# Optimization experiments

Measured on AMD Instinct MI355X. Metric: run time of the kernel, lower is better.

The kernel has to match this reference:

```python
import jax, jax.numpy as jnp
import numpy as np

B, C, H, W, NP = 4, 512, 32, 32, 2048
NH = 4
EPS = 1e-5


def setup_inputs() -> dict:
    key = jax.random.key(0)
    ks = jax.random.split(key, 12)
    s = 0.02
    d = {}
    d["img_feature"] = jax.random.normal(ks[0], (B, C, H, W), jnp.float32)
    d["point_feature"] = jax.random.normal(ks[1], (B, C, NP), jnp.float32)
    d["mlp_w1"] = jax.random.normal(ks[2], (2 * C, C), jnp.float32) * s
    d["mlp_b1"] = jnp.zeros((2 * C,), jnp.float32)
    d["bn1_gamma"] = jnp.ones((2 * C,), jnp.float32)
    d["bn1_beta"] = jnp.zeros((2 * C,), jnp.float32)
    d["bn1_mean"] = jnp.zeros((2 * C,), jnp.float32)
    d["bn1_var"] = jnp.ones((2 * C,), jnp.float32)
    d["mlp_w2"] = jax.random.normal(ks[3], (C, 2 * C), jnp.float32) * s
    d["mlp_b2"] = jnp.zeros((C,), jnp.float32)
    d["bn2_gamma"] = jnp.ones((C,), jnp.float32)
    d["bn2_beta"] = jnp.zeros((C,), jnp.float32)
    d["bn2_mean"] = jnp.zeros((C,), jnp.float32)
    d["bn2_var"] = jnp.ones((C,), jnp.float32)
    d["attn_qw"] = jax.random.normal(ks[4], (3, C, C), jnp.float32) * s
    d["attn_qb"] = jnp.zeros((3, C), jnp.float32)
    d["attn_kw"] = jax.random.normal(ks[5], (3, C, C), jnp.float32) * s
    d["attn_kb"] = jnp.zeros((3, C), jnp.float32)
    d["attn_vw"] = jax.random.normal(ks[6], (3, C, C), jnp.float32) * s
    d["attn_vb"] = jnp.zeros((3, C), jnp.float32)
    d["attn_ln_g"] = jnp.ones((3, C), jnp.float32)
    d["attn_ln_b"] = jnp.zeros((3, C), jnp.float32)
    return d


def _bn(x, g, b, m, v):  # x: [B, C, N], eval-mode batchnorm over channel dim
    return (x - m[:, None]) * jax.lax.rsqrt(v[:, None] + EPS) * g[:, None] + b[:, None]


def _mlp(x, w1, b1, g1, be1, m1, v1, w2, b2, g2, be2, m2, v2):
    # 1x1 Conv1d == per-position linear over channels
    y = jnp.einsum('oc,bcn->bon', w1, x) + b1[:, None]
    y = jax.nn.relu(_bn(y, g1, be1, m1, v1))
    z = jnp.einsum('oc,bcn->bon', w2, y) + b2[:, None]
    return jax.nn.relu(_bn(z, g2, be2, m2, v2))


def _self_attn(x, qw, qb, kw, kb, vw, vb, lng, lnb):
    # x: [B, S, E]; NOTE: original scales by 1/sqrt(hidden_size), not head_dim
    Bq, S, E = x.shape
    Hd = E // NH
    q = (jnp.einsum('bse,de->bsd', x, qw) + qb).reshape(Bq, S, NH, Hd)
    k = (jnp.einsum('bse,de->bsd', x, kw) + kb).reshape(Bq, S, NH, Hd)
    v = (jnp.einsum('bse,de->bsd', x, vw) + vb).reshape(Bq, S, NH, Hd)
    scores = jnp.einsum('bqhd,bkhd->bhqk', q, k) * (float(E) ** -0.5)
    attn = jax.nn.softmax(scores, axis=-1)
    out = jnp.einsum('bhqk,bkhd->bqhd', attn, v).reshape(Bq, S, E)
    y = out + x
    mu = jnp.mean(y, axis=-1, keepdims=True)
    var = jnp.var(y, axis=-1, keepdims=True)
    return (y - mu) * jax.lax.rsqrt(var + EPS) * lng + lnb


def reference(img_feature, point_feature, mlp_w1, mlp_b1, bn1_gamma, bn1_beta,
              bn1_mean, bn1_var, mlp_w2, mlp_b2, bn2_gamma, bn2_beta, bn2_mean,
              bn2_var, attn_qw, attn_qb, attn_kw, attn_kb, attn_vw, attn_vb,
              attn_ln_g, attn_ln_b):
    b, c, h, w = img_feature.shape
    i_in = img_feature.reshape(b, c, h * w)  # [B, C, N_i]
    mlp_args = (mlp_w1, mlp_b1, bn1_gamma, bn1_beta, bn1_mean, bn1_var,
                mlp_w2, mlp_b2, bn2_gamma, bn2_beta, bn2_mean, bn2_var)
    p_feat = _mlp(point_feature, *mlp_args)  # [B, C, N_p]
    i_feat = _mlp(i_in, *mlp_args)           # [B, C, N_i]
    phi = jnp.einsum('bcp,bci->bpi', p_feat, i_feat) * (float(c) ** -0.5)
    phi_p = jax.nn.softmax(phi, axis=1)   # softmax over points
    phi_i = jax.nn.softmax(phi, axis=-1)  # softmax over image positions
    I_enh = jnp.einsum('bcp,bpi->bci', p_feat, phi_p)  # [B, C, N_i]
    P_enh = jnp.einsum('bci,bpi->bcp', i_feat, phi_i)  # [B, C, N_p]
    att = lambda x, j: _self_attn(x, attn_qw[j], attn_qb[j], attn_kw[j],
                                  attn_kb[j], attn_vw[j], attn_vb[j],
                                  attn_ln_g[j], attn_ln_b[j])
    I = att(jnp.swapaxes(I_enh, 1, 2), 0)  # [B, N_i, C]
    P = att(jnp.swapaxes(P_enh, 1, 2), 1)  # [B, N_p, C]
    joint = jnp.concatenate([P, I], axis=1)  # [B, N_p + N_i, C]
    return att(joint, 2)
```

## Files before the change

### kernel.cpp

```cpp
#include <hip/hip_runtime.h>
#include <math.h>

#define LN_EPS 1e-5f

typedef __attribute__((ext_vector_type(8))) short bf16x8;
typedef __attribute__((ext_vector_type(4))) float f32x4;

#define GLDS16(g, l) __builtin_amdgcn_global_load_lds( \
    (const __attribute__((address_space(1))) unsigned int*)(g), \
    (__attribute__((address_space(3))) unsigned int*)(l), 16, 0, 0)

__device__ __forceinline__ float b2f(unsigned short h) { return __uint_as_float(((unsigned)h) << 16); }
__device__ __forceinline__ unsigned short f2b(float f) {
  unsigned u = __float_as_uint(f);
  unsigned r = (u + 0x7fffu + ((u >> 16) & 1u)) >> 16;
  return (unsigned short)r;
}
__device__ __forceinline__ float ld(const float* p) { return *p; }
__device__ __forceinline__ float ld(const unsigned short* p) { return b2f(*p); }
__device__ __forceinline__ void st(float* p, float v) { *p = v; }
__device__ __forceinline__ void st(unsigned short* p, float v) { *p = f2b(v); }

__device__ __forceinline__ float bred_sum(float v, float* red) {
  for (int o = 32; o; o >>= 1) v += __shfl_down(v, o, 64);
  int wid = threadIdx.x >> 6;
  __syncthreads();
  if ((threadIdx.x & 63) == 0) red[wid] = v;
  __syncthreads();
  return red[0] + red[1] + red[2] + red[3];
}

__global__ void prep_all(
    const float* __restrict__ w1, const float* __restrict__ w2, const float* __restrict__ vw,
    const float* __restrict__ qw, const float* __restrict__ qb,
    const float* __restrict__ kw, const float* __restrict__ kb,
    const float* __restrict__ b1, const float* __restrict__ g1, const float* __restrict__ be1,
    const float* __restrict__ m1, const float* __restrict__ v1,
    const float* __restrict__ b2, const float* __restrict__ g2, const float* __restrict__ be2,
    const float* __restrict__ m2, const float* __restrict__ v2,
    unsigned short* __restrict__ w1b, unsigned short* __restrict__ w2b,
    unsigned short* __restrict__ vwb, unsigned short* __restrict__ qkw,
    float* __restrict__ qkbias, float* __restrict__ s1, float* __restrict__ f1,
    float* __restrict__ s2, float* __restrict__ f2)
{
  const float scl = 0.044194173824159216f * 1.4426950408889634f;
  int idx = blockIdx.x * 256 + threadIdx.x;
  {
    int j = idx >> 19; int r = idx & 524287; int n = r >> 9; int k = r & 511;
    float v = (n < 512) ? qw[j * 262144 + n * 512 + k] * scl
                        : kw[j * 262144 + (n - 512) * 512 + k];
    qkw[idx] = f2b(v);
  }
  if (idx < 524288) { w1b[idx] = f2b(w1[idx]); w2b[idx] = f2b(w2[idx]); }
  if (idx < 786432) vwb[idx] = f2b(vw[idx]);
  if (idx < 3072) {
    int j = idx >> 10, n = idx & 1023;
    qkbias[idx] = (n < 512) ? qb[j * 512 + n] * scl : kb[j * 512 + n - 512];
  }
  if (idx < 1024) { float s = g1[idx] * rsqrtf(v1[idx] + LN_EPS); s1[idx] = s; f1[idx] = (b1[idx] - m1[idx]) * s + be1[idx]; }
  if (idx < 512)  { float s = g2[idx] * rsqrtf(v2[idx] + LN_EPS); s2[idx] = s; f2[idx] = (b2[idx] - m2[idx]) * s + be2[idx]; }
}

template<typename TS, typename TD>
__global__ __launch_bounds__(256) void transpose_t(const TS* __restrict__ src,
    TD* __restrict__ dst, int R, int Cc, long sS, long sD) {
  __shared__ float t[32][33];
  src += (long)blockIdx.z * sS; dst += (long)blockIdx.z * sD;
  int c0 = blockIdx.x * 32, r0 = blockIdx.y * 32;
  int tx = threadIdx.x & 31, ty = threadIdx.x >> 5;
#pragma unroll
  for (int rr = 0; rr < 32; rr += 8) t[ty + rr][tx] = ld(&src[(long)(r0 + ty + rr) * Cc + c0 + tx]);
  __syncthreads();
#pragma unroll
  for (int rr = 0; rr < 32; rr += 8) st(&dst[(long)(c0 + ty + rr) * R + r0 + tx], t[tx][ty + rr]);
}

template<int PER>
__global__ __launch_bounds__(256) void softmax_k(const float* __restrict__ x,
    unsigned short* __restrict__ y, long bstr) {
  __shared__ float red[4];
  const int L = PER * 256;
  int b = blockIdx.y, r = blockIdx.x, tid = threadIdx.x;
  const float* p = x + (long)b * bstr + (long)r * L;
  unsigned short* o = y + (long)b * bstr + (long)r * L;
  float vals[PER];
  float mx = -1e30f;
#pragma unroll
  for (int t = 0; t < PER; t++) { float v = p[tid + (t << 8)]; vals[t] = v; mx = fmaxf(mx, v); }
  for (int ofs = 32; ofs; ofs >>= 1) mx = fmaxf(mx, __shfl_down(mx, ofs, 64));
  int wid = tid >> 6;
  if ((tid & 63) == 0) red[wid] = mx;
  __syncthreads();
  mx = fmaxf(fmaxf(red[0], red[1]), fmaxf(red[2], red[3]));
  float sm = 0.f;
#pragma unroll
  for (int t = 0; t < PER; t++) { float e = __expf(vals[t] - mx); vals[t] = e; sm += e; }
  sm = bred_sum(sm, red);
  float inv = 1.f / sm;
#pragma unroll
  for (int t = 0; t < PER; t++) o[tid + (t << 8)] = f2b(vals[t] * inv);
}

template<int EPI, typename TC>
__global__ __launch_bounds__(256) void gemm_bf16(
    const unsigned short* __restrict__ A, long sA, int lda,
    const unsigned short* __restrict__ B, long sB, int ldb,
    TC* __restrict__ C, long sC, int ldc,
    int M, int N, int K,
    const float* __restrict__ sc, const float* __restrict__ bi, float cscale)
{
  __shared__ short As[128 * 64];
  __shared__ short Bs[128 * 64];
  const int tid = threadIdx.x;
  const int lane = tid & 63, wid = tid >> 6;
  const int wm = wid >> 1, wn = wid & 1;
  const int l15 = lane & 15, l4 = lane >> 4, l7 = lane & 7;
  const int bm = blockIdx.y * 128, bn = blockIdx.x * 128;
  const int srow = lane >> 3;
  A += (long)blockIdx.z * sA; B += (long)blockIdx.z * sB; C += (long)blockIdx.z * sC;
  f32x4 acc[4][4] = {};
  for (int k0 = 0; k0 < K; k0 += 64) {
#pragma unroll
    for (int i = 0; i < 4; i++) {
      int row = (wid * 4 + i) * 8 + srow;
      int gcol = (l7 ^ (row & 7)) * 8;
      GLDS16(A + (long)(bm + row) * lda + k0 + gcol, &As[(wid * 4 + i) * 512]);
      GLDS16(B + (long)(bn + row) * ldb + k0 + gcol, &Bs[(wid * 4 + i) * 512]);
    }
    __syncthreads();
#pragma unroll
    for (int ks = 0; ks < 2; ks++) {
      bf16x8 af[4], bfr[4];
#pragma unroll
      for (int t = 0; t < 4; t++) {
        int ra = wm * 64 + t * 16 + l15;
        int rb = wn * 64 + t * 16 + l15;
        int ch = (l4 + 4 * ks) ^ (l15 & 7);
        af[t]  = *(const bf16x8*)&As[ra * 64 + ch * 8];
        bfr[t] = *(const bf16x8*)&Bs[rb * 64 + ch * 8];
      }
#pragma unroll
      for (int i = 0; i < 4; i++)
#pragma unroll
        for (int j2 = 0; j2 < 4; j2++)
          acc[i][j2] = __builtin_amdgcn_mfma_f32_16x16x32_bf16(af[i], bfr[j2], acc[i][j2], 0, 0, 0);
    }
    __syncthreads();
  }
#pragma unroll
  for (int i = 0; i < 4; i++) {
#pragma unroll
    for (int j2 = 0; j2 < 4; j2++) {
      int n = bn + wn * 64 + j2 * 16 + l15;
#pragma unroll
      for (int j = 0; j < 4; j++) {
        int m = bm + wm * 64 + i * 16 + l4 * 4 + j;
        float v = acc[i][j2][j];
        if (EPI == 1) v = fmaxf(fmaf(v, sc[n], bi[n]), 0.f);
        if (EPI == 2) v *= cscale;
        if (EPI == 3) v += bi[n];
        if (EPI == 4) v += bi[m];
        st(&C[(long)m * ldc + n], v);
      }
    }
  }
}

__global__ __launch_bounds__(512) void attn_flash(
    const unsigned short* __restrict__ qk, const unsigned short* __restrict__ vT,
    unsigned short* __restrict__ out, int S)
{
  __shared__ short Ks[64 * 128];
  __shared__ short Vs[128 * 64];
  __shared__ short Ps[8][1024];
  const int tid = threadIdx.x, lane = tid & 63, wid = tid >> 6;
  const int h = blockIdx.y, b = blockIdx.z;
  const int l15 = lane & 15, l4 = lane >> 4, l7 = l15 & 7;
  const long qkb = (long)b * S * 1024;
  const long vbb = (long)b * 512 * S;
  const long obase = (long)b * S * 512;
  const int qr0 = blockIdx.x * 128 + wid * 16;
  const int kR0 = tid >> 4, kC0 = tid & 15;
  const int kR1 = (tid + 512) >> 4, kC1 = tid & 15;
  const int vR0 = tid >> 3, vC0 = tid & 7;
  const int vR1 = (tid + 512) >> 3, vC1 = tid & 7;
  bf16x8 qf[4];
#pragma unroll
  for (int ks = 0; ks < 4; ks++)
    qf[ks] = *(const bf16x8*)(qk + qkb + (long)(qr0 + l15) * 1024 + h * 128 + l4 * 8 + ks * 32);
  f32x4 O[8] = {};
  float m_run = -1e30f, l_run = 0.f;
  const int NT = S >> 6;
  int4 kr0, kr1, vr0, vr1;
  auto load_regs = [&](int kt) {
    kr0 = *(const int4*)(qk + qkb + (long)(kt * 64 + kR0) * 1024 + 512 + h * 128 + kC0 * 8);
    kr1 = *(const int4*)(qk + qkb + (long)(kt * 64 + kR1) * 1024 + 512 + h * 128 + kC1 * 8);
    vr0 = *(const int4*)(vT + vbb + (long)(h * 128 + vR0) * S + kt * 64 + vC0 * 8);
    vr1 = *(const int4*)(vT + vbb + (long)(h * 128 + vR1) * S + kt * 64 + vC1 * 8);
  };
  load_regs(0);
  for (int kt = 0; kt < NT; kt++) {
    __syncthreads();
    *(int4*)&Ks[kR0 * 128 + ((kC0 ^ (kR0 & 7)) << 3)] = kr0;
    *(int4*)&Ks[kR1 * 128 + ((kC1 ^ (kR1 & 7)) << 3)] = kr1;
    *(int4*)&Vs[vR0 * 64 + ((vC0 ^ (vR0 & 7)) << 3)] = vr0;
    *(int4*)&Vs[vR1 * 64 + ((vC1 ^ (vR1 & 7)) << 3)] = vr1;
    __syncthreads();
    if (kt + 1 < NT) load_regs(kt + 1);
    f32x4 sacc[4] = {};
    __builtin_amdgcn_s_setprio(1);
#pragma unroll
    for (int f = 0; f < 4; f++) {
      int row = f * 16 + l15;
#pragma unroll
      for (int ks = 0; ks < 4; ks++) {
        bf16x8 kf = *(const bf16x8*)&Ks[row * 128 + (((l4 + 4 * ks) ^ l7) << 3)];
        sacc[f] = __builtin_amdgcn_mfma_f32_16x16x32_bf16(kf, qf[ks], sacc[f], 0, 0, 0);
      }
    }
    __builtin_amdgcn_s_setprio(0);
    float pmax = -1e30f;
#pragma unroll
    for (int f = 0; f < 4; f++)
#pragma unroll
      for (int j = 0; j < 4; j++) pmax = fmaxf(pmax, sacc[f][j]);
    pmax = fmaxf(pmax, __shfl_xor(pmax, 16, 64));
    pmax = fmaxf(pmax, __shfl_xor(pmax, 32, 64));
    if (!__all(pmax - m_run <= 8.f)) {
      float m_new = fmaxf(m_run, pmax);
      float corr = __builtin_exp2f(m_run - m_new);
      l_run *= corr; m_run = m_new;
#pragma unroll
      for (int fd = 0; fd < 8; fd++) {
        O[fd][0] *= corr; O[fd][1] *= corr; O[fd][2] *= corr; O[fd][3] *= corr;
      }
    }
    float ts = 0.f;
#pragma unroll
    for (int f = 0; f < 4; f++) {
      ushort4 pw;
#pragma unroll
      for (int j = 0; j < 4; j++) {
        float e = __builtin_exp2f(sacc[f][j] - m_run);
        ts += e;
        ((unsigned short*)&pw)[j] = f2b(e);
      }
      *(ushort4*)&Ps[wid][l15 * 64 + (((2 * f + (l4 >> 1)) ^ l7) << 3) + (l4 & 1) * 4] = pw;
    }
    ts += __shfl_xor(ts, 16, 64);
    ts += __shfl_xor(ts, 32, 64);
    l_run += ts;
    __builtin_amdgcn_s_setprio(1);
#pragma unroll
    for (int ks = 0; ks < 2; ks++) {
      int pch = ((l4 + 4 * ks) ^ l7) << 3;
      bf16x8 pf = *(const bf16x8*)&Ps[wid][l15 * 64 + pch];
#pragma unroll
      for (int fd = 0; fd < 8; fd++) {
        bf16x8 vf = *(const bf16x8*)&Vs[(fd * 16 + l15) * 64 + pch];
        O[fd] = __builtin_amdgcn_mfma_f32_16x16x32_bf16(vf, pf, O[fd], 0, 0, 0);
      }
    }
    __builtin_amdgcn_s_setprio(0);
  }
  float inv = 1.f / l_run;
  unsigned short* op = out + obase + (long)(qr0 + l15) * 512 + h * 128;
#pragma unroll
  for (int fd = 0; fd < 8; fd++) {
    ushort4 ov;
    ov.x = f2b(O[fd][0] * inv);
    ov.y = f2b(O[fd][1] * inv);
    ov.z = f2b(O[fd][2] * inv);
    ov.w = f2b(O[fd][3] * inv);
    *(ushort4*)&op[fd * 16 + l4 * 4] = ov;
  }
}

template<typename TD>
__global__ __launch_bounds__(256) void add_ln(
    const unsigned short* __restrict__ att, const unsigned short* __restrict__ resid,
    const float* __restrict__ g, const float* __restrict__ bt,
    TD* __restrict__ dst, long db, int S)
{
  __shared__ float red[4];
  int b = blockIdx.y, s = blockIdx.x, tid = threadIdx.x;
  const unsigned short* ap = att + ((long)b * S + s) * 512;
  const unsigned short* rp = resid + ((long)b * S + s) * 512;
  float y0 = b2f(ap[tid]) + b2f(rp[tid]);
  float y1 = b2f(ap[tid + 256]) + b2f(rp[tid + 256]);
  float mu = bred_sum(y0 + y1, red) * (1.f / 512.f);
  float d0 = y0 - mu, d1 = y1 - mu;
  float var = bred_sum(d0 * d0 + d1 * d1, red) * (1.f / 512.f);
  float rsv = rsqrtf(var + LN_EPS);
  TD* dp = dst + (long)b * db + (long)s * 512;
  st(&dp[tid], d0 * rsv * g[tid] + bt[tid]);
  st(&dp[tid + 256], d1 * rsv * g[tid + 256] + bt[tid + 256]);
}

extern "C" void kernel_launch(void* const* d_in, const int* in_sizes, int n_in,
                              void* d_out, int out_size, void* d_ws, size_t ws_size,
                              hipStream_t stream) {
  (void)in_sizes; (void)n_in; (void)out_size; (void)ws_size;
  const float* img = (const float*)d_in[0];
  const float* pts = (const float*)d_in[1];
  const float* w1  = (const float*)d_in[2];
  const float* b1  = (const float*)d_in[3];
  const float* g1  = (const float*)d_in[4];
  const float* be1 = (const float*)d_in[5];
  const float* m1  = (const float*)d_in[6];
  const float* v1  = (const float*)d_in[7];
  const float* w2  = (const float*)d_in[8];
  const float* b2  = (const float*)d_in[9];
  const float* g2  = (const float*)d_in[10];
  const float* be2 = (const float*)d_in[11];
  const float* m2  = (const float*)d_in[12];
  const float* v2  = (const float*)d_in[13];
  const float* qw  = (const float*)d_in[14];
  const float* qb  = (const float*)d_in[15];
  const float* kw  = (const float*)d_in[16];
  const float* kb  = (const float*)d_in[17];
  const float* vw  = (const float*)d_in[18];
  const float* vb  = (const float*)d_in[19];
  const float* lng = (const float*)d_in[20];
  const float* lnb = (const float*)d_in[21];
  float* out = (float*)d_out;
  float* ws  = (float*)d_ws;
  typedef unsigned short u16;

  u16*   xTu   = (u16*)ws;
  float* phi   = ws;
  u16*   y1u   = (u16*)(ws + 8388608);
  float* phiT  = ws + 8388608;
  u16*   featu = (u16*)(ws + 16777216);
  u16*   featTu= (u16*)(ws + 19922944);
  u16*   smI   = (u16*)(ws + 23068672);
  u16*   smPT  = (u16*)(ws + 27262976);
  u16*   Xi    = (u16*)(ws + 31457280);
  u16*   Xp    = (u16*)(ws + 32505856);
  u16*   jointu= (u16*)(ws + 34603008);
  u16*   w1b   = (u16*)(ws + 37748736);
  u16*   w2b   = (u16*)(ws + 38010880);
  u16*   qkwb  = (u16*)(ws + 38273024);
  u16*   vwb   = (u16*)(ws + 39059456);
  float* s1f   = ws + 39452672;
  float* f1f   = s1f + 1024;
  float* s2f   = f1f + 1024;
  float* f2f   = s2f + 512;
  float* qkbf  = ws + 39455744;
  u16*   qkbu  = (u16*)ws;
  u16*   vTu   = (u16*)(ws + 6291456);
  u16*   attu  = (u16*)(ws + 9437184);

  dim3 blk(256);
  prep_all<<<dim3(6144), blk, 0, stream>>>(w1, w2, vw, qw, qb, kw, kb,
      b1, g1, be1, m1, v1, b2, g2, be2, m2, v2,
      w1b, w2b, vwb, qkwb, qkbf, s1f, f1f, s2f, f2f);

  transpose_t<float, u16><<<dim3(64, 16, 4), blk, 0, stream>>>(pts, xTu, 512, 2048, 1048576L, 1572864L);
  transpose_t<float, u16><<<dim3(32, 16, 4), blk, 0, stream>>>(img, xTu + 1048576, 512, 1024, 524288L, 1572864L);

  gemm_bf16<1, u16><<<dim3(8, 24, 4), blk, 0, stream>>>(xTu, 1572864L, 512, w1b, 0L, 512,
      y1u, 3145728L, 1024, 3072, 1024, 512, s1f, f1f, 0.f);
  gemm_bf16<1, u16><<<dim3(4, 24, 4), blk, 0, stream>>>(y1u, 3145728L, 1024, w2b, 0L, 1024,
      featu, 1572864L, 512, 3072, 512, 1024, s2f, f2f, 0.f);
  transpose_t<u16, u16><<<dim3(16, 96, 4), blk, 0, stream>>>(featu, featTu, 3072, 512, 1572864L, 1572864L);
  gemm_bf16<2, float><<<dim3(8, 16, 4), blk, 0, stream>>>(featu, 1572864L, 512, featu + 1048576, 1572864L, 512,
      phi, 2097152L, 1024, 2048, 1024, 512, nullptr, nullptr, 0.044194173824159216f);
  transpose_t<float, float><<<dim3(32, 64, 4), blk, 0, stream>>>(phi, phiT, 2048, 1024, 2097152L, 2097152L);
  softmax_k<4><<<dim3(2048, 4), blk, 0, stream>>>(phi, smI, 2097152L);
  softmax_k<8><<<dim3(1024, 4), blk, 0, stream>>>(phiT, smPT, 2097152L);
  gemm_bf16<0, u16><<<dim3(4, 8, 4), blk, 0, stream>>>(smPT, 2097152L, 2048, featTu, 1572864L, 3072,
      Xi, 524288L, 512, 1024, 512, 2048, nullptr, nullptr, 0.f);
  gemm_bf16<0, u16><<<dim3(4, 16, 4), blk, 0, stream>>>(smI, 2097152L, 1024, featTu + 2048, 1572864L, 3072,
      Xp, 1048576L, 512, 2048, 512, 1024, nullptr, nullptr, 0.f);

  struct AttCfg { const u16* X; int S; int j; };
  AttCfg cfgs[3] = { {Xi, 1024, 0}, {Xp, 2048, 1}, {jointu, 3072, 2} };
  for (int a = 0; a < 3; a++) {
    const u16* X = cfgs[a].X; int S = cfgs[a].S; int j = cfgs[a].j;
    long xs = (long)S * 512;
    gemm_bf16<3, u16><<<dim3(8, S / 128, 4), blk, 0, stream>>>(X, xs, 512, qkwb + j * 524288, 0L, 512,
        qkbu, (long)S * 1024, 1024, S, 1024, 512, nullptr, qkbf + j * 1024, 0.f);
    gemm_bf16<4, u16><<<dim3(S / 128, 4, 4), blk, 0, stream>>>(vwb + j * 262144, 0L, 512, X, xs, 512,
        vTu, xs, S, 512, S, 512, nullptr, vb + j * 512, 0.f);
    attn_flash<<<dim3(S / 128, 4, 4), dim3(512), 0, stream>>>(qkbu, vTu, attu, S);
    if (a == 0)
      add_ln<u16><<<dim3(S, 4), blk, 0, stream>>>(attu, X, lng + j * 512, lnb + j * 512,
          jointu + 1048576, 1572864L, S);
    else if (a == 1)
      add_ln<u16><<<dim3(S, 4), blk, 0, stream>>>(attu, X, lng + j * 512, lnb + j * 512,
          jointu, 1572864L, S);
    else
      add_ln<float><<<dim3(S, 4), blk, 0, stream>>>(attu, X, lng + j * 512, lnb + j * 512,
          out, 1572864L, S);
  }
}
```

Before: 547.5 us.

## Fuse phi transpose into GEMM epilogue and compute softmax row sums via MFMA

The phi GEMM epilogue now also writes the transposed matrix directly, removing the separate fp32 transpose kernel and its full read/write pass. In the flash attention kernel, the running softmax denominator is accumulated by an extra MFMA against a vector of ones, replacing per-lane sums and cross-lane shuffles. The bf16 packing of the exponentials uses the hardware packed convert instruction. The transposed stores in the GEMM epilogue are strided and uncoalesced, and the denominator now comes from the bf16-rounded probabilities.

```diff
diff --git a/kernel.cpp b/kernel.cpp
--- a/kernel.cpp
+++ b/kernel.cpp
@@ -118,6 +118,8 @@
   const int bm = blockIdx.y * 128, bn = blockIdx.x * 128;
   const int srow = lane >> 3;
   A += (long)blockIdx.z * sA; B += (long)blockIdx.z * sB; C += (long)blockIdx.z * sC;
+  float* CT = nullptr;
+  if (EPI == 5) CT = (float*)bi + (long)blockIdx.z * sC;
   f32x4 acc[4][4] = {};
   for (int k0 = 0; k0 < K; k0 += 64) {
 #pragma unroll
@@ -160,6 +162,7 @@
         if (EPI == 2) v *= cscale;
         if (EPI == 3) v += bi[n];
         if (EPI == 4) v += bi[m];
+        if (EPI == 5) { v *= cscale; CT[(long)n * M + m] = v; }
         st(&C[(long)m * ldc + n], v);
       }
     }
@@ -188,8 +191,12 @@
 #pragma unroll
   for (int ks = 0; ks < 4; ks++)
     qf[ks] = *(const bf16x8*)(qk + qkb + (long)(qr0 + l15) * 1024 + h * 128 + l4 * 8 + ks * 32);
+  bf16x8 onev;
+#pragma unroll
+  for (int j = 0; j < 8; j++) onev[j] = (short)0x3F80;
   f32x4 O[8] = {};
-  float m_run = -1e30f, l_run = 0.f;
+  f32x4 Ol = {};
+  float m_run = -1e30f;
   const int NT = S >> 6;
   int4 kr0, kr1, vr0, vr1;
   auto load_regs = [&](int kt) {
@@ -219,42 +226,44 @@
       }
     }
     __builtin_amdgcn_s_setprio(0);
-    float pmax = -1e30f;
-#pragma unroll
-    for (int f = 0; f < 4; f++)
-#pragma unroll
-      for (int j = 0; j < 4; j++) pmax = fmaxf(pmax, sacc[f][j]);
+    float pmax = fmaxf(fmaxf(sacc[0][0], sacc[0][1]), sacc[0][2]);
+    pmax = fmaxf(fmaxf(pmax, sacc[0][3]), sacc[1][0]);
+    pmax = fmaxf(fmaxf(pmax, sacc[1][1]), sacc[1][2]);
+    pmax = fmaxf(fmaxf(pmax, sacc[1][3]), sacc[2][0]);
+    pmax = fmaxf(fmaxf(pmax, sacc[2][1]), sacc[2][2]);
+    pmax = fmaxf(fmaxf(pmax, sacc[2][3]), sacc[3][0]);
+    pmax = fmaxf(fmaxf(pmax, sacc[3][1]), sacc[3][2]);
+    pmax = fmaxf(pmax, sacc[3][3]);
     pmax = fmaxf(pmax, __shfl_xor(pmax, 16, 64));
     pmax = fmaxf(pmax, __shfl_xor(pmax, 32, 64));
     if (!__all(pmax - m_run <= 8.f)) {
       float m_new = fmaxf(m_run, pmax);
       float corr = __builtin_exp2f(m_run - m_new);
-      l_run *= corr; m_run = m_new;
+      m_run = m_new;
+      Ol[0] *= corr; Ol[1] *= corr; Ol[2] *= corr; Ol[3] *= corr;
 #pragma unroll
       for (int fd = 0; fd < 8; fd++) {
         O[fd][0] *= corr; O[fd][1] *= corr; O[fd][2] *= corr; O[fd][3] *= corr;
       }
     }
-    float ts = 0.f;
 #pragma unroll
     for (int f = 0; f < 4; f++) {
-      ushort4 pw;
-#pragma unroll
-      for (int j = 0; j < 4; j++) {
-        float e = __builtin_exp2f(sacc[f][j] - m_run);
-        ts += e;
-        ((unsigned short*)&pw)[j] = f2b(e);
-      }
-      *(ushort4*)&Ps[wid][l15 * 64 + (((2 * f + (l4 >> 1)) ^ l7) << 3) + (l4 & 1) * 4] = pw;
-    }
-    ts += __shfl_xor(ts, 16, 64);
-    ts += __shfl_xor(ts, 32, 64);
-    l_run += ts;
+      float e0 = __builtin_exp2f(sacc[f][0] - m_run);
+      float e1 = __builtin_exp2f(sacc[f][1] - m_run);
+      float e2 = __builtin_exp2f(sacc[f][2] - m_run);
+      float e3 = __builtin_exp2f(sacc[f][3] - m_run);
+      unsigned w0, w1;
+      asm("v_cvt_pk_bf16_f32 %0, %1, %2" : "=v"(w0) : "v"(e0), "v"(e1));
+      asm("v_cvt_pk_bf16_f32 %0, %1, %2" : "=v"(w1) : "v"(e2), "v"(e3));
+      int2 pw; pw.x = (int)w0; pw.y = (int)w1;
+      *(int2*)&Ps[wid][l15 * 64 + (((2 * f + (l4 >> 1)) ^ l7) << 3) + (l4 & 1) * 4] = pw;
+    }
     __builtin_amdgcn_s_setprio(1);
 #pragma unroll
     for (int ks = 0; ks < 2; ks++) {
       int pch = ((l4 + 4 * ks) ^ l7) << 3;
       bf16x8 pf = *(const bf16x8*)&Ps[wid][l15 * 64 + pch];
+      Ol = __builtin_amdgcn_mfma_f32_16x16x32_bf16(onev, pf, Ol, 0, 0, 0);
 #pragma unroll
       for (int fd = 0; fd < 8; fd++) {
         bf16x8 vf = *(const bf16x8*)&Vs[(fd * 16 + l15) * 64 + pch];
@@ -263,7 +272,7 @@
     }
     __builtin_amdgcn_s_setprio(0);
   }
-  float inv = 1.f / l_run;
+  float inv = 1.f / Ol[0];
   unsigned short* op = out + obase + (long)(qr0 + l15) * 512 + h * 128;
 #pragma unroll
   for (int fd = 0; fd < 8; fd++) {
@@ -364,9 +373,8 @@
   gemm_bf16<1, u16><<<dim3(4, 24, 4), blk, 0, stream>>>(y1u, 3145728L, 1024, w2b, 0L, 1024,
       featu, 1572864L, 512, 3072, 512, 1024, s2f, f2f, 0.f);
   transpose_t<u16, u16><<<dim3(16, 96, 4), blk, 0, stream>>>(featu, featTu, 3072, 512, 1572864L, 1572864L);
-  gemm_bf16<2, float><<<dim3(8, 16, 4), blk, 0, stream>>>(featu, 1572864L, 512, featu + 1048576, 1572864L, 512,
-      phi, 2097152L, 1024, 2048, 1024, 512, nullptr, nullptr, 0.044194173824159216f);
-  transpose_t<float, float><<<dim3(32, 64, 4), blk, 0, stream>>>(phi, phiT, 2048, 1024, 2097152L, 2097152L);
+  gemm_bf16<5, float><<<dim3(8, 16, 4), blk, 0, stream>>>(featu, 1572864L, 512, featu + 1048576, 1572864L, 512,
+      phi, 2097152L, 1024, 2048, 1024, 512, nullptr, (const float*)phiT, 0.044194173824159216f);
   softmax_k<4><<<dim3(2048, 4), blk, 0, stream>>>(phi, smI, 2097152L);
   softmax_k<8><<<dim3(1024, 4), blk, 0, stream>>>(phiT, smPT, 2097152L);
   gemm_bf16<0, u16><<<dim3(4, 8, 4), blk, 0, stream>>>(smPT, 2097152L, 2048, featTu, 1572864L, 3072,
```

Result: faster. 521.2 us (-4.8%).
